# Kernel optimization log

Measured on AMD Instinct MI355X. Metric: run time of the kernel, lower is better.

## Reference

```python
import jax, jax.numpy as jnp
import numpy as np

LEAK = 0.2

def setup_inputs() -> dict:
    key = jax.random.key(0)
    ks = jax.random.split(key, 8)
    B, D, H1, H2, F = 2048, 3072, 512, 256, 100
    s = lambda fan_in: 1.0 / np.sqrt(fan_in)
    return {
        "x":  jax.random.normal(ks[0], (B, D), dtype=jnp.float32),
        "W1": jax.random.uniform(ks[1], (D, H1), jnp.float32, -s(D), s(D)),
        "b1": jnp.zeros((H1,), jnp.float32),
        "W2": jax.random.uniform(ks[2], (H1, H2), jnp.float32, -s(H1), s(H1)),
        "b2": jnp.zeros((H2,), jnp.float32),
        "T":  jax.random.normal(ks[3], (H2, F), dtype=jnp.float32),
        "Wf": jax.random.uniform(ks[4], (H2 + F, 1), jnp.float32, -s(H2 + F), s(H2 + F)),
        "bf": jnp.zeros((1,), jnp.float32),
    }

def reference(x, W1, b1, W2, b2, T, Wf, bf):
    # MLP stack with LeakyReLU(0.2)
    h = jax.nn.leaky_relu(x @ W1 + b1, LEAK)          # (B,512)
    h = jax.nn.leaky_relu(h @ W2 + b2, LEAK)          # (B,256)
    # Minibatch discrimination: pairwise L1 per feature, exp, sum over batch
    m = h @ T                                          # (B,100)
    d = jnp.abs(m[:, None, :] - m[None, :, :])         # (B,B,100)
    feats = jnp.sum(jnp.exp(-d), axis=1)               # (B,100)
    z = jnp.concatenate([h, feats], axis=1)            # (B,356)
    return z @ Wf + bf                                 # (B,1)
```

## Files before the change

kernel.cpp:

```cpp
#include <hip/hip_runtime.h>
#include <hip/hip_bf16.h>

#define LEAK 0.2f

typedef __attribute__((ext_vector_type(8))) short short8;
typedef __attribute__((ext_vector_type(4))) float f32x4;

__global__ __launch_bounds__(256) void k_convert(const float* __restrict__ x,
                                                 __hip_bfloat16* __restrict__ xb, int n4) {
  int idx = blockIdx.x * 256 + threadIdx.x;
  if (idx >= n4) return;
  float4 v = reinterpret_cast<const float4*>(x)[idx];
  union { ushort4 u; __hip_bfloat16 h[4]; } c;
  c.h[0] = __float2bfloat16(v.x);
  c.h[1] = __float2bfloat16(v.y);
  c.h[2] = __float2bfloat16(v.z);
  c.h[3] = __float2bfloat16(v.w);
  reinterpret_cast<ushort4*>(xb)[idx] = c.u;
}

__global__ __launch_bounds__(256) void k_transpose(const float* __restrict__ W,
                                                   __hip_bfloat16* __restrict__ Wt,
                                                   int K, int N) {
  __shared__ float tile[32][33];
  int k0 = blockIdx.x * 32, n0 = blockIdx.y * 32;
  int tx = threadIdx.x, ty = threadIdx.y;
#pragma unroll
  for (int r = 0; r < 4; ++r) {
    int k = k0 + ty + r * 8;
    int n = n0 + tx;
    tile[ty + r * 8][tx] = (n < N) ? W[(long)k * N + n] : 0.f;
  }
  __syncthreads();
#pragma unroll
  for (int r = 0; r < 4; ++r) {
    int n = n0 + ty + r * 8;
    int k = k0 + tx;
    Wt[(long)n * K + k] = __float2bfloat16(tile[tx][ty + r * 8]);
  }
}

template <bool TRANSP>
__global__ __launch_bounds__(256) void k_gemm(const __hip_bfloat16* __restrict__ A,
                                              const __hip_bfloat16* __restrict__ Bt,
                                              float* __restrict__ Cp,
                                              int M, int N, int K, int KSPL, int ldO) {
  __shared__ __align__(16) __hip_bfloat16 As[64][40];
  __shared__ __align__(16) __hip_bfloat16 Bs[64][40];
  int tid = threadIdx.x;
  int lane = tid & 63;
  int wv = tid >> 6;
  int wm = wv & 1, wn = wv >> 1;
  int quad = lane >> 4, l16 = lane & 15;
  long m0 = (long)blockIdx.x * 64, n0 = (long)blockIdx.y * 64;
  int srow = tid >> 2, scol = (tid & 3) * 8;
  int kStart = blockIdx.z * KSPL;
  const __hip_bfloat16* Ag = A + (m0 + srow) * K + kStart + scol;
  const __hip_bfloat16* Bg = Bt + (n0 + srow) * K + kStart + scol;

  int4 ra = *reinterpret_cast<const int4*>(Ag);
  int4 rb = *reinterpret_cast<const int4*>(Bg);

  f32x4 acc[2][2] = {};
  for (int kb = 0; kb < KSPL; kb += 32) {
    *reinterpret_cast<int4*>(&As[srow][scol]) = ra;
    *reinterpret_cast<int4*>(&Bs[srow][scol]) = rb;
    __syncthreads();
    if (kb + 32 < KSPL) {
      ra = *reinterpret_cast<const int4*>(Ag + kb + 32);
      rb = *reinterpret_cast<const int4*>(Bg + kb + 32);
    }
    short8 af[2], bfr[2];
#pragma unroll
    for (int t = 0; t < 2; ++t) {
      af[t]  = *reinterpret_cast<const short8*>(&As[wm * 32 + t * 16 + l16][quad * 8]);
      bfr[t] = *reinterpret_cast<const short8*>(&Bs[wn * 32 + t * 16 + l16][quad * 8]);
    }
#pragma unroll
    for (int tm = 0; tm < 2; ++tm)
#pragma unroll
      for (int tn = 0; tn < 2; ++tn)
        acc[tm][tn] =
            __builtin_amdgcn_mfma_f32_16x16x32_bf16(af[tm], bfr[tn], acc[tm][tn], 0, 0, 0);
    __syncthreads();
  }

  float* Cz = Cp + (long)blockIdx.z * M * N;
#pragma unroll
  for (int tm = 0; tm < 2; ++tm)
#pragma unroll
    for (int tn = 0; tn < 2; ++tn)
#pragma unroll
      for (int r = 0; r < 4; ++r) {
        long gm = m0 + wm * 32 + tm * 16 + quad * 4 + r;
        long gn = n0 + wn * 32 + tn * 16 + l16;
        if (TRANSP) Cz[gn * ldO + gm] = acc[tm][tn][r];
        else        Cz[gm * ldO + gn] = acc[tm][tn][r];
      }
}

template <int NZ, bool OUTF>
__global__ __launch_bounds__(256) void k_comb(const float* __restrict__ P,
                                              const float* __restrict__ bias,
                                              float* __restrict__ Of,
                                              __hip_bfloat16* __restrict__ Ob,
                                              int total4, int nmask) {
  int idx = blockIdx.x * 256 + threadIdx.x;
  if (idx >= total4) return;
  float4 v = reinterpret_cast<const float4*>(P)[idx];
#pragma unroll
  for (int z = 1; z < NZ; ++z) {
    float4 a = reinterpret_cast<const float4*>(P + (long)z * total4 * 4)[idx];
    v.x += a.x; v.y += a.y; v.z += a.z; v.w += a.w;
  }
  int col = (idx * 4) & nmask;
  float4 bs = *reinterpret_cast<const float4*>(bias + col);
  v.x += bs.x; v.y += bs.y; v.z += bs.z; v.w += bs.w;
  v.x = v.x > 0.f ? v.x : LEAK * v.x;
  v.y = v.y > 0.f ? v.y : LEAK * v.y;
  v.z = v.z > 0.f ? v.z : LEAK * v.z;
  v.w = v.w > 0.f ? v.w : LEAK * v.w;
  if (OUTF) reinterpret_cast<float4*>(Of)[idx] = v;
  union { ushort4 u; __hip_bfloat16 h[4]; } c;
  c.h[0] = __float2bfloat16(v.x);
  c.h[1] = __float2bfloat16(v.y);
  c.h[2] = __float2bfloat16(v.z);
  c.h[3] = __float2bfloat16(v.w);
  reinterpret_cast<ushort4*>(Ob)[idx] = c.u;
}

__global__ __launch_bounds__(1024) void k_bucketfeats(const float* __restrict__ mTz,
                                                      float* __restrict__ featsT) {
  __shared__ float sP[2048], sN[2048];
  __shared__ float Sp[2048], Sn[2048];
  __shared__ int Smeta[2048];
  __shared__ short sB[2048];
  __shared__ int cnt[256], bstart[256], bcur[256];
  __shared__ float bsP[256], bsN[256], Pbel[256], Nab[256];
  __shared__ float wred[32];
  __shared__ float sMin, sMax;
  int f = blockIdx.x;
  int t = threadIdx.x;
  int lane = t & 63, wv = t >> 6;
  const long FS = 2048L * 128;
  const float* row = mTz + (long)f * 2048;

  float m[2];
  float lmin = 3.4e38f, lmax = -3.4e38f;
#pragma unroll
  for (int r = 0; r < 2; ++r) {
    int e = t + r * 1024;
    float v = row[e] + row[FS + e] + row[2 * FS + e] + row[3 * FS + e];
    m[r] = v;
    lmin = fminf(lmin, v);
    lmax = fmaxf(lmax, v);
  }
#pragma unroll
  for (int d = 32; d; d >>= 1) {
    lmin = fminf(lmin, __shfl_down(lmin, d));
    lmax = fmaxf(lmax, __shfl_down(lmax, d));
  }
  if (lane == 0) { wred[wv] = lmin; wred[16 + wv] = lmax; }
  if (t < 256) cnt[t] = 0;
  __syncthreads();
  if (t == 0) {
    float a = wred[0], b = wred[16];
    for (int i = 1; i < 16; ++i) { a = fminf(a, wred[i]); b = fmaxf(b, wred[16 + i]); }
    sMin = a; sMax = b;
  }
  __syncthreads();
  float mn = sMin, mx = sMax;
  float rge = mx - mn;
  float scale = (rge > 1e-20f) ? 255.0f / rge : 0.f;
  float mid = 0.5f * (mn + mx);
#pragma unroll
  for (int r = 0; r < 2; ++r) {
    int e = t + r * 1024;
    float v = m[r];
    int b = (int)((v - mn) * scale);
    b = b < 255 ? b : 255;
    float arg = fminf(fmaxf(v - mid, -60.f), 60.f);
    sP[e] = __expf(arg);
    sN[e] = __expf(-arg);
    sB[e] = (short)b;
    atomicAdd(&cnt[b], 1);
  }
  __syncthreads();
  if (wv == 0) {
    int b4 = lane * 4;
    int c0 = cnt[b4], c1 = cnt[b4 + 1], c2 = cnt[b4 + 2], c3 = cnt[b4 + 3];
    int tot = c0 + c1 + c2 + c3;
    int inc = tot;
#pragma unroll
    for (int d = 1; d < 64; d <<= 1) {
      int y = __shfl_up(inc, d);
      if (lane >= d) inc += y;
    }
    int run = inc - tot;
    bstart[b4] = run; bcur[b4] = run; run += c0;
    bstart[b4 + 1] = run; bcur[b4 + 1] = run; run += c1;
    bstart[b4 + 2] = run; bcur[b4 + 2] = run; run += c2;
    bstart[b4 + 3] = run; bcur[b4 + 3] = run;
  }
  __syncthreads();
#pragma unroll
  for (int r = 0; r < 2; ++r) {
    int e = t + r * 1024;
    int b = sB[e];
    int slot = atomicAdd(&bcur[b], 1);
    Sp[slot] = sP[e];
    Sn[slot] = sN[e];
    Smeta[slot] = (b << 16) | e;
  }
  __syncthreads();
  if (t < 256) {
    int s0 = bstart[t], s1 = s0 + cnt[t];
    float ap = 0.f, an = 0.f;
    for (int q = s0; q < s1; ++q) { ap += Sp[q]; an += Sn[q]; }
    bsP[t] = ap; bsN[t] = an;
  }
  __syncthreads();
  if (wv == 0) {
    int b4 = lane * 4;
    float p0 = bsP[b4], p1 = bsP[b4 + 1], p2 = bsP[b4 + 2], p3 = bsP[b4 + 3];
    float n0 = bsN[b4], n1 = bsN[b4 + 1], n2 = bsN[b4 + 2], n3 = bsN[b4 + 3];
    float tp = p0 + p1 + p2 + p3, tn = n0 + n1 + n2 + n3;
    float ip = tp, in_ = tn;
#pragma unroll
    for (int d = 1; d < 64; d <<= 1) {
      float yp = __shfl_up(ip, d);
      float yn = __shfl_up(in_, d);
      if (lane >= d) { ip += yp; in_ += yn; }
    }
    float totn = __shfl(in_, 63);
    float runp = ip - tp;
    float runn = in_ - tn;
    Pbel[b4] = runp; Nab[b4] = totn - runn - n0; runp += p0; runn += n0;
    Pbel[b4 + 1] = runp; Nab[b4 + 1] = totn - runn - n1; runp += p1; runn += n1;
    Pbel[b4 + 2] = runp; Nab[b4 + 2] = totn - runn - n2; runp += p2; runn += n2;
    Pbel[b4 + 3] = runp; Nab[b4 + 3] = totn - runn - n3;
  }
  __syncthreads();
#pragma unroll
  for (int r = 0; r < 2; ++r) {
    int s = t + r * 1024;
    int meta = Smeta[s];
    int b = meta >> 16;
    int idx = meta & 0xFFFF;
    float p = Sp[s], n = Sn[s];
    float acc = n * Pbel[b] + p * Nab[b];
    int q0 = bstart[b], q1 = q0 + cnt[b];
    for (int q = q0; q < q1; ++q) acc += fminf(p * Sn[q], n * Sp[q]);
    featsT[(long)f * 2048 + idx] = acc;
  }
}

__global__ __launch_bounds__(256) void k_final(const float* __restrict__ h2f,
                                               const float* __restrict__ featsT,
                                               const float* __restrict__ Wf,
                                               const float* __restrict__ bfp,
                                               float* __restrict__ out) {
  int wv = threadIdx.x >> 6, lane = threadIdx.x & 63;
  long i = (long)blockIdx.x * 4 + wv;
  const float* hrow = h2f + i * 256;
  float s = 0.f;
#pragma unroll
  for (int c = lane; c < 256; c += 64) s += hrow[c] * Wf[c];
  for (int f = lane; f < 100; f += 64) s += featsT[(long)f * 2048 + i] * Wf[256 + f];
#pragma unroll
  for (int off = 32; off; off >>= 1) s += __shfl_down(s, off);
  if (lane == 0) out[i] = s + bfp[0];
}

extern "C" void kernel_launch(void* const* d_in, const int* in_sizes, int n_in,
                              void* d_out, int out_size, void* d_ws, size_t ws_size,
                              hipStream_t stream) {
  const float* x  = (const float*)d_in[0];
  const float* W1 = (const float*)d_in[1];
  const float* b1 = (const float*)d_in[2];
  const float* W2 = (const float*)d_in[3];
  const float* b2 = (const float*)d_in[4];
  const float* T  = (const float*)d_in[5];
  const float* Wf = (const float*)d_in[6];
  const float* bf = (const float*)d_in[7];
  float* out = (float*)d_out;

  char* w = (char*)d_ws;
  auto alloc = [&](size_t b) { char* p = w; w += (b + 255) & ~(size_t)255; return p; };
  char*           xbr  = alloc(2048L * 3072 * 2);
  __hip_bfloat16* xb   = (__hip_bfloat16*)xbr;
  float*          P2   = (float*)xbr;
  float*          P3   = (float*)(xbr + 4194304);
  float*          feT  = (float*)(xbr + 8388608);
  __hip_bfloat16* W1t  = (__hip_bfloat16*)alloc(512L * 3072 * 2);
  __hip_bfloat16* W2t  = (__hip_bfloat16*)alloc(256L * 512 * 2);
  __hip_bfloat16* Tt   = (__hip_bfloat16*)alloc(128L * 256 * 2);
  __hip_bfloat16* h1b  = (__hip_bfloat16*)alloc(2048L * 512 * 2);
  float*          h2f  = (float*)alloc(2048L * 256 * 4);
  __hip_bfloat16* h2b  = (__hip_bfloat16*)alloc(2048L * 256 * 2);
  float*          P1   = (float*)alloc(3L * 2048 * 512 * 4);

  k_convert<<<6144, 256, 0, stream>>>(x, xb, 1572864);
  k_transpose<<<dim3(96, 16), dim3(32, 8), 0, stream>>>(W1, W1t, 3072, 512);
  k_transpose<<<dim3(16, 8),  dim3(32, 8), 0, stream>>>(W2, W2t, 512, 256);
  k_transpose<<<dim3(8, 4),   dim3(32, 8), 0, stream>>>(T,  Tt,  256, 100);
  k_gemm<false><<<dim3(32, 8, 3), 256, 0, stream>>>(xb, W1t, P1, 2048, 512, 3072, 1024, 512);
  k_comb<3, false><<<1024, 256, 0, stream>>>(P1, b1, nullptr, h1b, 262144, 511);
  k_gemm<false><<<dim3(32, 4, 2), 256, 0, stream>>>(h1b, W2t, P2, 2048, 256, 512, 256, 256);
  k_comb<2, true><<<512, 256, 0, stream>>>(P2, b2, h2f, h2b, 131072, 255);
  k_gemm<true><<<dim3(32, 2, 4), 256, 0, stream>>>(h2b, Tt, P3, 2048, 128, 256, 64, 2048);
  k_bucketfeats<<<100, 1024, 0, stream>>>(P3, feT);
  k_final<<<512, 256, 0, stream>>>(h2f, feT, Wf, bf, out);
}
```

Before: 138.1 us.

## Fuse prep kernels into one launch and deepen GEMM K-tile to 64

Merges the x conversion and three weight transposes into a single k_prep launch, indexed by a flattened block range. The GEMM K-step grows from 32 to 64, with two 16-byte loads per operand per thread and two MFMA half-steps per tile. This halves the barrier count and loop iterations and enlarges each global fetch. Workspace buffers P2, P3 and feT no longer alias xb, which costs extra memory but avoids reuse hazards. LDS per block grows and all GEMM K splits must now be multiples of 64.

New measurement: 127.0 us. -8.1%, faster.

```diff
diff --git a/kernel.cpp b/kernel.cpp
--- a/kernel.cpp
+++ b/kernel.cpp
@@ -6,38 +6,55 @@
 typedef __attribute__((ext_vector_type(8))) short short8;
 typedef __attribute__((ext_vector_type(4))) float f32x4;
 
-__global__ __launch_bounds__(256) void k_convert(const float* __restrict__ x,
-                                                 __hip_bfloat16* __restrict__ xb, int n4) {
-  int idx = blockIdx.x * 256 + threadIdx.x;
-  if (idx >= n4) return;
-  float4 v = reinterpret_cast<const float4*>(x)[idx];
-  union { ushort4 u; __hip_bfloat16 h[4]; } c;
-  c.h[0] = __float2bfloat16(v.x);
-  c.h[1] = __float2bfloat16(v.y);
-  c.h[2] = __float2bfloat16(v.z);
-  c.h[3] = __float2bfloat16(v.w);
-  reinterpret_cast<ushort4*>(xb)[idx] = c.u;
-}
-
-__global__ __launch_bounds__(256) void k_transpose(const float* __restrict__ W,
-                                                   __hip_bfloat16* __restrict__ Wt,
-                                                   int K, int N) {
+__global__ __launch_bounds__(256) void k_prep(const float* __restrict__ x,
+                                              __hip_bfloat16* __restrict__ xb,
+                                              const float* __restrict__ W1,
+                                              __hip_bfloat16* __restrict__ W1t,
+                                              const float* __restrict__ W2,
+                                              __hip_bfloat16* __restrict__ W2t,
+                                              const float* __restrict__ T,
+                                              __hip_bfloat16* __restrict__ Tt) {
+  int b = blockIdx.x;
+  int t = threadIdx.x;
+  if (b < 6144) {
+    int idx = b * 256 + t;
+    float4 v = reinterpret_cast<const float4*>(x)[idx];
+    union { ushort4 u; __hip_bfloat16 h[4]; } c;
+    c.h[0] = __float2bfloat16(v.x);
+    c.h[1] = __float2bfloat16(v.y);
+    c.h[2] = __float2bfloat16(v.z);
+    c.h[3] = __float2bfloat16(v.w);
+    reinterpret_cast<ushort4*>(xb)[idx] = c.u;
+    return;
+  }
   __shared__ float tile[32][33];
-  int k0 = blockIdx.x * 32, n0 = blockIdx.y * 32;
-  int tx = threadIdx.x, ty = threadIdx.y;
+  const float* W;
+  __hip_bfloat16* Wt;
+  int K, N, kblk, nblk;
+  int b2 = b - 6144;
+  if (b2 < 1536) {
+    W = W1; Wt = W1t; K = 3072; N = 512;
+    kblk = b2 % 96; nblk = b2 / 96;
+  } else if (b2 < 1664) {
+    int b3 = b2 - 1536;
+    W = W2; Wt = W2t; K = 512; N = 256;
+    kblk = b3 % 16; nblk = b3 / 16;
+  } else {
+    int b4 = b2 - 1664;
+    W = T; Wt = Tt; K = 256; N = 100;
+    kblk = b4 % 8; nblk = b4 / 8;
+  }
+  int k0 = kblk * 32, n0 = nblk * 32;
+  int tx = t & 31, ty = t >> 5;
 #pragma unroll
   for (int r = 0; r < 4; ++r) {
-    int k = k0 + ty + r * 8;
     int n = n0 + tx;
-    tile[ty + r * 8][tx] = (n < N) ? W[(long)k * N + n] : 0.f;
-  }
-  __syncthreads();
-#pragma unroll
-  for (int r = 0; r < 4; ++r) {
-    int n = n0 + ty + r * 8;
-    int k = k0 + tx;
-    Wt[(long)n * K + k] = __float2bfloat16(tile[tx][ty + r * 8]);
-  }
+    tile[ty + r * 8][tx] = (n < N) ? W[(long)(k0 + ty + r * 8) * N + n] : 0.f;
+  }
+  __syncthreads();
+#pragma unroll
+  for (int r = 0; r < 4; ++r)
+    Wt[(long)(n0 + ty + r * 8) * K + k0 + tx] = __float2bfloat16(tile[tx][ty + r * 8]);
 }
 
 template <bool TRANSP>
@@ -45,43 +62,52 @@
                                               const __hip_bfloat16* __restrict__ Bt,
                                               float* __restrict__ Cp,
                                               int M, int N, int K, int KSPL, int ldO) {
-  __shared__ __align__(16) __hip_bfloat16 As[64][40];
-  __shared__ __align__(16) __hip_bfloat16 Bs[64][40];
+  __shared__ __align__(16) __hip_bfloat16 As[64][72];
+  __shared__ __align__(16) __hip_bfloat16 Bs[64][72];
   int tid = threadIdx.x;
   int lane = tid & 63;
   int wv = tid >> 6;
   int wm = wv & 1, wn = wv >> 1;
   int quad = lane >> 4, l16 = lane & 15;
   long m0 = (long)blockIdx.x * 64, n0 = (long)blockIdx.y * 64;
-  int srow = tid >> 2, scol = (tid & 3) * 8;
+  int srow = tid >> 2, scol = (tid & 3) * 16;
   int kStart = blockIdx.z * KSPL;
   const __hip_bfloat16* Ag = A + (m0 + srow) * K + kStart + scol;
   const __hip_bfloat16* Bg = Bt + (n0 + srow) * K + kStart + scol;
 
-  int4 ra = *reinterpret_cast<const int4*>(Ag);
-  int4 rb = *reinterpret_cast<const int4*>(Bg);
+  int4 ra0 = *reinterpret_cast<const int4*>(Ag);
+  int4 ra1 = *reinterpret_cast<const int4*>(Ag + 8);
+  int4 rb0 = *reinterpret_cast<const int4*>(Bg);
+  int4 rb1 = *reinterpret_cast<const int4*>(Bg + 8);
 
   f32x4 acc[2][2] = {};
-  for (int kb = 0; kb < KSPL; kb += 32) {
-    *reinterpret_cast<int4*>(&As[srow][scol]) = ra;
-    *reinterpret_cast<int4*>(&Bs[srow][scol]) = rb;
+  for (int kb = 0; kb < KSPL; kb += 64) {
+    *reinterpret_cast<int4*>(&As[srow][scol]) = ra0;
+    *reinterpret_cast<int4*>(&As[srow][scol + 8]) = ra1;
+    *reinterpret_cast<int4*>(&Bs[srow][scol]) = rb0;
+    *reinterpret_cast<int4*>(&Bs[srow][scol + 8]) = rb1;
     __syncthreads();
-    if (kb + 32 < KSPL) {
-      ra = *reinterpret_cast<const int4*>(Ag + kb + 32);
-      rb = *reinterpret_cast<const int4*>(Bg + kb + 32);
+    if (kb + 64 < KSPL) {
+      ra0 = *reinterpret_cast<const int4*>(Ag + kb + 64);
+      ra1 = *reinterpret_cast<const int4*>(Ag + kb + 72);
+      rb0 = *reinterpret_cast<const int4*>(Bg + kb + 64);
+      rb1 = *reinterpret_cast<const int4*>(Bg + kb + 72);
     }
-    short8 af[2], bfr[2];
-#pragma unroll
-    for (int t = 0; t < 2; ++t) {
-      af[t]  = *reinterpret_cast<const short8*>(&As[wm * 32 + t * 16 + l16][quad * 8]);
-      bfr[t] = *reinterpret_cast<const short8*>(&Bs[wn * 32 + t * 16 + l16][quad * 8]);
+#pragma unroll
+    for (int half = 0; half < 2; ++half) {
+      short8 af[2], bfr[2];
+#pragma unroll
+      for (int t = 0; t < 2; ++t) {
+        af[t]  = *reinterpret_cast<const short8*>(&As[wm * 32 + t * 16 + l16][half * 32 + quad * 8]);
+        bfr[t] = *reinterpret_cast<const short8*>(&Bs[wn * 32 + t * 16 + l16][half * 32 + quad * 8]);
+      }
+#pragma unroll
+      for (int tm = 0; tm < 2; ++tm)
+#pragma unroll
+        for (int tn = 0; tn < 2; ++tn)
+          acc[tm][tn] =
+              __builtin_amdgcn_mfma_f32_16x16x32_bf16(af[tm], bfr[tn], acc[tm][tn], 0, 0, 0);
     }
-#pragma unroll
-    for (int tm = 0; tm < 2; ++tm)
-#pragma unroll
-      for (int tn = 0; tn < 2; ++tn)
-        acc[tm][tn] =
-            __builtin_amdgcn_mfma_f32_16x16x32_bf16(af[tm], bfr[tn], acc[tm][tn], 0, 0, 0);
     __syncthreads();
   }
 
@@ -287,23 +313,19 @@
 
   char* w = (char*)d_ws;
   auto alloc = [&](size_t b) { char* p = w; w += (b + 255) & ~(size_t)255; return p; };
-  char*           xbr  = alloc(2048L * 3072 * 2);
-  __hip_bfloat16* xb   = (__hip_bfloat16*)xbr;
-  float*          P2   = (float*)xbr;
-  float*          P3   = (float*)(xbr + 4194304);
-  float*          feT  = (float*)(xbr + 8388608);
-  __hip_bfloat16* W1t  = (__hip_bfloat16*)alloc(512L * 3072 * 2);
-  __hip_bfloat16* W2t  = (__hip_bfloat16*)alloc(256L * 512 * 2);
-  __hip_bfloat16* Tt   = (__hip_bfloat16*)alloc(128L * 256 * 2);
-  __hip_bfloat16* h1b  = (__hip_bfloat16*)alloc(2048L * 512 * 2);
-  float*          h2f  = (float*)alloc(2048L * 256 * 4);
-  __hip_bfloat16* h2b  = (__hip_bfloat16*)alloc(2048L * 256 * 2);
-  float*          P1   = (float*)alloc(3L * 2048 * 512 * 4);
-
-  k_convert<<<6144, 256, 0, stream>>>(x, xb, 1572864);
-  k_transpose<<<dim3(96, 16), dim3(32, 8), 0, stream>>>(W1, W1t, 3072, 512);
-  k_transpose<<<dim3(16, 8),  dim3(32, 8), 0, stream>>>(W2, W2t, 512, 256);
-  k_transpose<<<dim3(8, 4),   dim3(32, 8), 0, stream>>>(T,  Tt,  256, 100);
+  __hip_bfloat16* xb  = (__hip_bfloat16*)alloc(2048L * 3072 * 2);
+  __hip_bfloat16* W1t = (__hip_bfloat16*)alloc(512L * 3072 * 2);
+  __hip_bfloat16* W2t = (__hip_bfloat16*)alloc(256L * 512 * 2);
+  __hip_bfloat16* Tt  = (__hip_bfloat16*)alloc(128L * 256 * 2);
+  __hip_bfloat16* h1b = (__hip_bfloat16*)alloc(2048L * 512 * 2);
+  float*          h2f = (float*)alloc(2048L * 256 * 4);
+  __hip_bfloat16* h2b = (__hip_bfloat16*)alloc(2048L * 256 * 2);
+  float*          feT = (float*)alloc(100L * 2048 * 4);
+  float*          P1  = (float*)alloc(3L * 2048 * 512 * 4);
+  float*          P2  = (float*)alloc(2L * 2048 * 256 * 4);
+  float*          P3  = (float*)alloc(4L * 2048 * 128 * 4);
+
+  k_prep<<<7840, 256, 0, stream>>>(x, xb, W1, W1t, W2, W2t, T, Tt);
   k_gemm<false><<<dim3(32, 8, 3), 256, 0, stream>>>(xb, W1t, P1, 2048, 512, 3072, 1024, 512);
   k_comb<3, false><<<1024, 256, 0, stream>>>(P1, b1, nullptr, h1b, 262144, 511);
   k_gemm<false><<<dim3(32, 4, 2), 256, 0, stream>>>(h1b, W2t, P2, 2048, 256, 512, 256, 256);
```
